# Kernel tuning notes

Measured on AMD Instinct MI355X. Metric: run time of the kernel, lower is better.

Reference implementation:

```python
import jax, jax.numpy as jnp
import numpy as np

D_MODEL = 512
NUM_HEADS = 8
HEAD_DIM = 64  # D_MODEL // NUM_HEADS


def setup_inputs() -> dict:
    key = jax.random.key(0)
    kq, kk, kv, kw, kb = jax.random.split(key, 5)
    B, S = 2, 2048
    query = jax.random.normal(kq, (B, S, D_MODEL), dtype=jnp.float32)
    key_t = jax.random.normal(kk, (B, S, D_MODEL), dtype=jnp.float32)
    value = jax.random.normal(kv, (B, S, D_MODEL), dtype=jnp.float32)
    # shared projection (nn.Linear(d_models, d_models)) applied to q, k, v
    scale = 1.0 / np.sqrt(D_MODEL)
    W = jax.random.uniform(kw, (D_MODEL, D_MODEL), dtype=jnp.float32, minval=-scale, maxval=scale)
    b = jax.random.uniform(kb, (D_MODEL,), dtype=jnp.float32, minval=-scale, maxval=scale)
    return {"query": query, "key": key_t, "value": value, "W": W, "b": b}


def reference(query, key, value, W, b):
    B, S, _ = query.shape
    H, Dh = NUM_HEADS, HEAD_DIM

    def proj(x):  # nn.Linear + ReLU, shared across q/k/v
        return jax.nn.relu(jnp.einsum('bsd,ed->bse', x, W) + b)

    # [B, S, d] -> [B, H, S, Dh]
    split = lambda x: proj(x).reshape(B, S, H, Dh).transpose(0, 2, 1, 3)
    Q, K, V = split(query), split(key), split(value)

    scores = jnp.einsum('bhqd,bhkd->bhqk', Q, K) / jnp.sqrt(jnp.float32(Dh))
    causal_mask = jnp.triu(jnp.ones((S, S), dtype=bool), k=1)  # True above diagonal
    scores = jnp.where(causal_mask, -jnp.inf, scores)
    attn = jax.nn.softmax(scores, axis=-1)
    out = jnp.einsum('bhqk,bhkd->bhqd', attn, V)  # [B, H, S, Dh]

    # faithful to original: transpose(0,1) swaps batch and heads, then view
    final = jnp.swapaxes(out, 0, 1).reshape(B, -1, D_MODEL)  # [B, S, d_model]
    return final
```

## Files before the change

### kernel.cpp

```cpp
#include <hip/hip_runtime.h>
#include <hip/hip_bf16.h>
#include <cstdint>
#include <cstddef>

typedef __bf16 bf16_t;
typedef bf16_t bf16x8 __attribute__((ext_vector_type(8)));
typedef float f32x4 __attribute__((ext_vector_type(4)));
typedef float f32x16 __attribute__((ext_vector_type(16)));
typedef unsigned short u16;
typedef u16 u16x8 __attribute__((ext_vector_type(8)));

#define S_LEN 2048
#define NB 2
#define NH 8
#define DHD 64
#define DM 512

static __device__ __forceinline__ u16 bfbits(float f) {
  union { __bf16 h; u16 u; } c; c.h = (__bf16)f; return c.u;
}
static __device__ __forceinline__ float bits2f(u16 b) {
  union { u16 u; __bf16 h; } c; c.u = b; return (float)c.h;
}
static __device__ __forceinline__ uint32_t pkbf(float a, float b) {
  union { __bf16 h[2]; uint32_t u; } c;
  c.h[0] = (__bf16)a; c.h[1] = (__bf16)b;
  return c.u;
}
static __device__ __forceinline__ void gload16(const void* g, void* l) {
  __builtin_amdgcn_global_load_lds(
      (const __attribute__((address_space(1))) uint32_t*)g,
      (__attribute__((address_space(3))) uint32_t*)l, 16, 0, 0);
}

static __device__ __forceinline__ int slot_of(int bh, int t32, int chunk) {
  int qb = t32 >> 2;
  int nc = (2 * (qb + 1) + 9) / 10;
  int off;
  if (qb < 10) off = (qb - 5) * 8;
  else if (qb < 15) off = 40 + (qb - 10) * 12;
  else off = 100;
  return bh * 116 + off + (t32 & 3) * nc + chunk;
}

__launch_bounds__(256, 3)
__global__ void proj_kernel(const float* __restrict__ Xq, const float* __restrict__ Xk,
                            const float* __restrict__ Xv, const float* __restrict__ W,
                            const float* __restrict__ bias,
                            u16* __restrict__ Qw, u16* __restrict__ Kw,
                            u16* __restrict__ Vt64) {
  __shared__ __align__(16) char pool[49152];
  float* AB[2]; float* BB[2];
  AB[0] = (float*)pool;
  AB[1] = AB[0] + 4096;
  BB[0] = AB[1] + 4096;
  BB[1] = BB[0] + 2048;

  const int bid = blockIdx.x;
  const int xcd = bid & 7;
  const int u = bid >> 3;
  const int n0 = (u & 7) * 64;
  const int mi = u >> 3;
  const int mg = (xcd * 12 + mi) * 128;
  const int z = mg >> 12;
  const int m_in = mg & 4095;
  const int b = m_in >> 11;
  const int s0m = m_in & (S_LEN - 1);
  const int hh = n0 >> 6;
  const float* __restrict__ X = (z == 0) ? Xq : ((z == 1) ? Xk : Xv);
  X += (size_t)m_in * DM;

  const int t = threadIdx.x;
  const int lane = t & 63;
  const int wid = t >> 6;
  const int wr = wid >> 1, wc = wid & 1;
  const int fr = lane & 15, fg = lane >> 4;

  f32x4 acc[4][2] = {};

  const int lrow = lane >> 3;
  const int lblk = lane & 7;

  auto stage = [&](int bf, int k0) {
    #pragma unroll
    for (int i = 0; i < 4; ++i) {
      int c = wid * 4 + i;
      int r = c * 8 + lrow;
      gload16(X + (size_t)r * DM + k0 + ((lblk ^ (r & 7)) << 2), AB[bf] + c * 256);
    }
    #pragma unroll
    for (int i = 0; i < 2; ++i) {
      int c = wid * 2 + i;
      int r = c * 8 + lrow;
      gload16(W + (size_t)(n0 + r) * DM + k0 + ((lblk ^ (r & 7)) << 2), BB[bf] + c * 256);
    }
  };

  stage(0, 0);
  int cb = 0;
  for (int t16 = 0; t16 < 16; ++t16) {
    __syncthreads();
    if (t16 < 15) stage(cb ^ 1, (t16 + 1) * 32);
    const float* Ac = AB[cb];
    const float* Bc = BB[cb];
    bf16x8 af[4], bfr[2];
    #pragma unroll
    for (int m2 = 0; m2 < 4; ++m2) {
      int r = wr*64 + m2*16 + fr;
      f32x4 lo = *(const f32x4*)&Ac[r*32 + (((2*fg)     ^ (r & 7)) << 2)];
      f32x4 hi = *(const f32x4*)&Ac[r*32 + (((2*fg + 1) ^ (r & 7)) << 2)];
      union { u16x8 s; bf16x8 v; } f;
      f.s[0]=bfbits(lo[0]); f.s[1]=bfbits(lo[1]); f.s[2]=bfbits(lo[2]); f.s[3]=bfbits(lo[3]);
      f.s[4]=bfbits(hi[0]); f.s[5]=bfbits(hi[1]); f.s[6]=bfbits(hi[2]); f.s[7]=bfbits(hi[3]);
      af[m2] = f.v;
    }
    #pragma unroll
    for (int ni = 0; ni < 2; ++ni) {
      int r = wc*32 + ni*16 + fr;
      f32x4 lo = *(const f32x4*)&Bc[r*32 + (((2*fg)     ^ (r & 7)) << 2)];
      f32x4 hi = *(const f32x4*)&Bc[r*32 + (((2*fg + 1) ^ (r & 7)) << 2)];
      union { u16x8 s; bf16x8 v; } f;
      f.s[0]=bfbits(lo[0]); f.s[1]=bfbits(lo[1]); f.s[2]=bfbits(lo[2]); f.s[3]=bfbits(lo[3]);
      f.s[4]=bfbits(hi[0]); f.s[5]=bfbits(hi[1]); f.s[6]=bfbits(hi[2]); f.s[7]=bfbits(hi[3]);
      bfr[ni] = f.v;
    }
    __builtin_amdgcn_s_setprio(1);
    #pragma unroll
    for (int m2 = 0; m2 < 4; ++m2)
      #pragma unroll
      for (int ni = 0; ni < 2; ++ni)
        acc[m2][ni] = __builtin_amdgcn_mfma_f32_16x16x32_bf16(af[m2], bfr[ni], acc[m2][ni], 0, 0, 0);
    __builtin_amdgcn_s_setprio(0);
    cb ^= 1;
  }
  __syncthreads();

  const float QSCALE = 0.125f * 1.44269504089f;
  const size_t bhh = (size_t)(b * NH + hh);
  u16* epi = (u16*)pool;

  if (z == 2) {
    #pragma unroll
    for (int m2 = 0; m2 < 4; ++m2) {
      #pragma unroll
      for (int ni = 0; ni < 2; ++ni) {
        int e = wc*32 + ni*16 + fr;
        int m = wr*64 + m2*16 + fg*4;
        float bv = bias[n0 + e];
        float v0 = fmaxf(acc[m2][ni][0] + bv, 0.f);
        float v1 = fmaxf(acc[m2][ni][1] + bv, 0.f);
        float v2 = fmaxf(acc[m2][ni][2] + bv, 0.f);
        float v3 = fmaxf(acc[m2][ni][3] + bv, 0.f);
        uint2 w; w.x = pkbf(v0, v1); w.y = pkbf(v2, v3);
        *(uint2*)&epi[e*136 + m] = w;
      }
    }
    __syncthreads();
    const int e = t >> 2, mc = (t & 3) * 32;
    const int sb = (s0m >> 6) + (mc >> 6);
    u16* dst = Vt64 + (((size_t)bhh * 32 + sb) * 64 + e) * 64 + (mc & 63);
    #pragma unroll
    for (int i = 0; i < 4; ++i)
      *(uint4*)(dst + i*8) = *(const uint4*)&epi[e*136 + mc + i*8];
  } else {
    #pragma unroll
    for (int m2 = 0; m2 < 4; ++m2) {
      #pragma unroll
      for (int ni = 0; ni < 2; ++ni) {
        int e = wc*32 + ni*16 + fr;
        float bv = bias[n0 + e];
        #pragma unroll
        for (int r = 0; r < 4; ++r) {
          float v = acc[m2][ni][r] + bv;
          if (z == 0) v *= QSCALE;
          v = fmaxf(v, 0.f);
          epi[(wr*64 + m2*16 + fg*4 + r)*72 + e] = bfbits(v);
        }
      }
    }
    __syncthreads();
    const int mrow = t >> 1, ec = (t & 1) * 32;
    u16* dst = ((z == 0) ? Qw : Kw) + (bhh * S_LEN + s0m + mrow) * DHD + ec;
    #pragma unroll
    for (int i = 0; i < 4; ++i)
      *(uint4*)(dst + i*8) = *(const uint4*)&epi[mrow*72 + ec + i*8];
  }
}

static __device__ const uint8_t QBT[34] = {4,5,6,7,8,9,9,10,10,11,11,12,12,13,13,14,14,14,15,15,15,
                                           3,8,13, 2,7,12, 1,6,11, 0,5,10,15};
static __device__ const uint8_t CKT[34] = {0,0,0,0,0,0,1,0,1,0,1,0,1,0,1,0,1,2,0,1,2,
                                           0,1,2, 0,1,2, 0,1,2, 0,1,2,3};

__launch_bounds__(256, 3)
__global__ void attn_kernel(const u16* __restrict__ Qw, const u16* __restrict__ Kw,
                            const u16* __restrict__ Vt64, u16* __restrict__ Opart,
                            float* __restrict__ lbuf, float* __restrict__ out) {
  __shared__ u16 KLDS[2][4096];
  __shared__ u16 VLDS[2][4096];
  const int t = threadIdx.x;
  const int lane = t & 63;
  const int wid = t >> 6;
  const int lam = lane & 31;
  const int hi = lane >> 5;
  const int h8 = hi << 3, h4 = hi << 2;
  const int bid = blockIdx.x;
  const int bh = bid & 15;
  const int u = bid >> 4;
  const int qb = QBT[u], chunk = CKT[u];
  const int steps_total = (qb + 1) * 2;
  const int sc0 = chunk * 10;
  const int sc1e = sc0 + 10;
  const int sc1 = (sc1e < steps_total) ? sc1e : steps_total;
  const int t32 = qb * 4 + wid;
  const int q0 = qb * 128 + wid * 32;

  const u16* __restrict__ Qh = Qw + (size_t)bh * S_LEN * DHD;
  const u16* __restrict__ Kh = Kw + (size_t)bh * S_LEN * DHD;
  const u16* __restrict__ V64 = Vt64 + (size_t)bh * 32 * 64 * 64;

  bf16x8 qf[4];
  #pragma unroll
  for (int c = 0; c < 4; ++c)
    qf[c] = *(const bf16x8*)(Qh + (size_t)(q0 + lam) * DHD + c*16 + h8);

  const int lrow = lane >> 3;
  const int lblk = lane & 7;
  auto stage = [&](int bf, int s) {
    #pragma unroll
    for (int i = 0; i < 2; ++i) {
      int c = wid * 2 + i;
      int r = c * 8 + lrow;
      int sw = (lblk ^ (r & 7)) << 3;
      gload16(Kh + (size_t)(s * 64 + r) * 64 + sw, &KLDS[bf][c * 512]);
      gload16(V64 + ((size_t)s * 64 + r) * 64 + sw, &VLDS[bf][c * 512]);
    }
  };

  f32x16 o0 = {}, o1 = {};
  float lsum = 0.f;

  auto softpack = [&](const f32x16& sc, bool msk, bf16x8& pb0v, bf16x8& pb1v) {
    float p[16];
    #pragma unroll
    for (int r = 0; r < 16; ++r) {
      float ev = __builtin_amdgcn_exp2f(sc[r]);
      int kc = (r & 3) + ((r >> 2) << 3) + h4;
      if (msk && kc > lam) ev = 0.f;
      p[r] = ev;
      lsum += ev;
    }
    uint32_t X0 = pkbf(p[0], p[1]),  X1 = pkbf(p[2], p[3]);
    uint32_t X2 = pkbf(p[4], p[5]),  X3 = pkbf(p[6], p[7]);
    uint32_t X4 = pkbf(p[8], p[9]),  X5 = pkbf(p[10], p[11]);
    uint32_t X6 = pkbf(p[12], p[13]), X7 = pkbf(p[14], p[15]);
    asm("v_permlane32_swap_b32 %0, %1" : "+v"(X0), "+v"(X2));
    asm("v_permlane32_swap_b32 %0, %1" : "+v"(X1), "+v"(X3));
    asm("v_permlane32_swap_b32 %0, %1" : "+v"(X4), "+v"(X6));
    asm("v_permlane32_swap_b32 %0, %1" : "+v"(X5), "+v"(X7));
    union U8 { uint32_t u[4]; bf16x8 v; };
    U8 a, bU;
    a.u[0] = X0; a.u[1] = X1; a.u[2] = X2; a.u[3] = X3;
    bU.u[0] = X4; bU.u[1] = X5; bU.u[2] = X6; bU.u[3] = X7;
    pb0v = a.v; pb1v = bU.v;
  };

  stage(0, sc0);
  int cb = 0;
  for (int s = sc0; s < sc1; ++s) {
    __syncthreads();
    if (s + 1 < sc1) stage(cb ^ 1, s + 1);
    const int d2 = t32 - 2 * s;
    bf16x8 a0, a1, b0v, b1v;
    f32x16 sA = {}, sB = {};
    if (d2 >= 0) {
      bf16x8 kA[4];
      #pragma unroll
      for (int c = 0; c < 4; ++c) {
        int r = lam, e = ((2*c + hi) ^ (r & 7)) * 8;
        kA[c] = *(const bf16x8*)&KLDS[cb][r*64 + e];
      }
      __builtin_amdgcn_s_setprio(1);
      #pragma unroll
      for (int c = 0; c < 4; ++c)
        sA = __builtin_amdgcn_mfma_f32_32x32x16_bf16(kA[c], qf[c], sA, 0, 0, 0);
      __builtin_amdgcn_s_setprio(0);
    }
    if (d2 >= 1) {
      bf16x8 kB[4];
      #pragma unroll
      for (int c = 0; c < 4; ++c) {
        int r = 32 + lam, e = ((2*c + hi) ^ (r & 7)) * 8;
        kB[c] = *(const bf16x8*)&KLDS[cb][r*64 + e];
      }
      __builtin_amdgcn_s_setprio(1);
      #pragma unroll
      for (int c = 0; c < 4; ++c)
        sB = __builtin_amdgcn_mfma_f32_32x32x16_bf16(kB[c], qf[c], sB, 0, 0, 0);
      __builtin_amdgcn_s_setprio(0);
    }
    if (d2 >= 0) softpack(sA, d2 == 0, a0, a1);
    if (d2 >= 1) softpack(sB, d2 == 1, b0v, b1v);
    if (d2 >= 0) {
      bf16x8 v0[2], v1[2];
      #pragma unroll
      for (int c2 = 0; c2 < 2; ++c2) {
        int r0 = lam,      e0 = ((2*c2 + hi) ^ (r0 & 7)) * 8;
        int r1 = 32 + lam, e1 = ((2*c2 + hi) ^ (r1 & 7)) * 8;
        v0[c2] = *(const bf16x8*)&VLDS[cb][r0*64 + e0];
        v1[c2] = *(const bf16x8*)&VLDS[cb][r1*64 + e1];
      }
      __builtin_amdgcn_s_setprio(1);
      o0 = __builtin_amdgcn_mfma_f32_32x32x16_bf16(v0[0], a0, o0, 0, 0, 0);
      o0 = __builtin_amdgcn_mfma_f32_32x32x16_bf16(v0[1], a1, o0, 0, 0, 0);
      o1 = __builtin_amdgcn_mfma_f32_32x32x16_bf16(v1[0], a0, o1, 0, 0, 0);
      o1 = __builtin_amdgcn_mfma_f32_32x32x16_bf16(v1[1], a1, o1, 0, 0, 0);
      __builtin_amdgcn_s_setprio(0);
    }
    if (d2 >= 1) {
      bf16x8 v0[2], v1[2];
      #pragma unroll
      for (int c2 = 0; c2 < 2; ++c2) {
        int r0 = lam,      e0 = ((4 + 2*c2 + hi) ^ (r0 & 7)) * 8;
        int r1 = 32 + lam, e1 = ((4 + 2*c2 + hi) ^ (r1 & 7)) * 8;
        v0[c2] = *(const bf16x8*)&VLDS[cb][r0*64 + e0];
        v1[c2] = *(const bf16x8*)&VLDS[cb][r1*64 + e1];
      }
      __builtin_amdgcn_s_setprio(1);
      o0 = __builtin_amdgcn_mfma_f32_32x32x16_bf16(v0[0], b0v, o0, 0, 0, 0);
      o0 = __builtin_amdgcn_mfma_f32_32x32x16_bf16(v0[1], b1v, o0, 0, 0, 0);
      o1 = __builtin_amdgcn_mfma_f32_32x32x16_bf16(v1[0], b0v, o1, 0, 0, 0);
      o1 = __builtin_amdgcn_mfma_f32_32x32x16_bf16(v1[1], b1v, o1, 0, 0, 0);
      __builtin_amdgcn_s_setprio(0);
    }
    cb ^= 1;
  }

  float l = lsum + __shfl_xor(lsum, 32);

  if (qb <= 4) {
    const int b = bh >> 3, hh = bh & 7;
    const float inv = 1.0f / l;
    float* orow = out + (((size_t)(hh * NB + b)) * S_LEN + (q0 + lam)) * DHD;
    #pragma unroll
    for (int r = 0; r < 16; ++r) {
      int d = (r & 3) + ((r >> 2) << 3) + h4;
      orow[d] = o0[r] * inv;
      orow[d + 32] = o1[r] * inv;
    }
  } else {
    const int slot = slot_of(bh, t32, chunk);
    uint32_t w[16] __attribute__((aligned(16)));
    #pragma unroll
    for (int m = 0; m < 8; ++m) {
      w[m]     = pkbf(o0[2*m], o0[2*m+1]);
      w[8 + m] = pkbf(o1[2*m], o1[2*m+1]);
    }
    u16* op = Opart + (size_t)slot * 2048 + (size_t)lane * 32;
    #pragma unroll
    for (int i = 0; i < 4; ++i)
      *(uint4*)(op + i*8) = *(const uint4*)&w[i*4];
    if (lane < 32) lbuf[slot * 32 + lane] = l;
  }
}

__launch_bounds__(256)
__global__ void reduce_kernel(const u16* __restrict__ Opart,
                              const float* __restrict__ lbuf,
                              float* __restrict__ out) {
  const int t = threadIdx.x;
  const int unit = blockIdx.x * 4 + (t >> 6);
  const int bh = unit & 15;
  const int ti = 20 + (unit >> 4);
  const int qb = ti >> 2;
  const int nc = (2 * (qb + 1) + 9) / 10;
  const int lane = t & 63;
  const int lam = lane & 31;
  const int h4 = (lane >> 5) << 2;
  const int slot0 = slot_of(bh, ti, 0);

  float O[32];
  #pragma unroll
  for (int i = 0; i < 32; ++i) O[i] = 0.f;
  float L = 0.f;

  for (int c = 0; c < nc; ++c) {
    const u16* op = Opart + (size_t)(slot0 + c) * 2048 + (size_t)lane * 32;
    L += lbuf[(slot0 + c) * 32 + lam];
    #pragma unroll
    for (int i = 0; i < 4; ++i) {
      uint4 v = *(const uint4*)(op + i*8);
      uint32_t a[4] = {v.x, v.y, v.z, v.w};
      #pragma unroll
      for (int jj = 0; jj < 4; ++jj) {
        O[i*8 + 2*jj]     += bits2f((u16)(a[jj] & 0xFFFFu));
        O[i*8 + 2*jj + 1] += bits2f((u16)(a[jj] >> 16));
      }
    }
  }

  const int b = bh >> 3, hh = bh & 7;
  const float inv = 1.0f / L;
  float* orow = out + (((size_t)(hh * NB + b)) * S_LEN + (ti*32 + lam)) * DHD;
  #pragma unroll
  for (int r = 0; r < 16; ++r) {
    int d = (r & 3) + ((r >> 2) << 3) + h4;
    orow[d] = O[r] * inv;
    orow[d + 32] = O[16 + r] * inv;
  }
}

extern "C" void kernel_launch(void* const* d_in, const int* in_sizes, int n_in,
                              void* d_out, int out_size, void* d_ws, size_t ws_size,
                              hipStream_t stream) {
  const float* q = (const float*)d_in[0];
  const float* k = (const float*)d_in[1];
  const float* v = (const float*)d_in[2];
  const float* W = (const float*)d_in[3];
  const float* b = (const float*)d_in[4];

  const size_t elems = (size_t)NB * NH * S_LEN * DHD;
  u16* Qw = (u16*)d_ws;
  u16* Kw = Qw + elems;
  u16* Vt64 = Kw + elems;
  u16* Opart = Vt64 + elems;
  float* lbuf = (float*)(Opart + (size_t)1856 * 2048);

  proj_kernel<<<dim3(768), dim3(256), 0, stream>>>(q, k, v, W, b, Qw, Kw, Vt64);

  attn_kernel<<<dim3(544), dim3(256), 0, stream>>>(Qw, Kw, Vt64, Opart, lbuf, (float*)d_out);

  reduce_kernel<<<dim3(176), dim3(256), 0, stream>>>(Opart, lbuf, (float*)d_out);
}
```

Measured before the change: 51.21 us.

## Pre-convert inputs and weight to bf16 and deepen the projection load pipeline

Adds a separate conversion kernel that turns q, k, v and W from fp32 into bf16 in workspace. The projection GEMM then stages bf16 tiles straight into LDS and skips the per-iteration fp32-to-bf16 conversion. Its LDS ring grows from two to four buffers, three stages in flight, with explicit vmcnt waits. The cost is an extra kernel launch plus a full fp32 read and bf16 write of all inputs. Opart is now aliased onto the converted-input buffer, which is safe because projection has finished before attention writes it.

```diff
diff --git a/kernel.cpp b/kernel.cpp
--- a/kernel.cpp
+++ b/kernel.cpp
@@ -43,19 +43,29 @@
   return bh * 116 + off + (t32 & 3) * nc + chunk;
 }
 
+__launch_bounds__(256)
+__global__ void cvt_kernel(const float* __restrict__ q, const float* __restrict__ k,
+                           const float* __restrict__ v, const float* __restrict__ W,
+                           u16* __restrict__ dst) {
+  const int z = blockIdx.y;
+  if (z == 3 && blockIdx.x >= 128) return;
+  const float* __restrict__ src = (z == 0) ? q : (z == 1) ? k : (z == 2) ? v : W;
+  u16* __restrict__ d = dst + (size_t)z * 2097152;
+  size_t i = ((size_t)blockIdx.x * 256 + threadIdx.x) * 8;
+  float4 a = *reinterpret_cast<const float4*>(src + i);
+  float4 b = *reinterpret_cast<const float4*>(src + i + 4);
+  u16x8 r;
+  r[0] = bfbits(a.x); r[1] = bfbits(a.y); r[2] = bfbits(a.z); r[3] = bfbits(a.w);
+  r[4] = bfbits(b.x); r[5] = bfbits(b.y); r[6] = bfbits(b.z); r[7] = bfbits(b.w);
+  *reinterpret_cast<u16x8*>(d + i) = r;
+}
+
 __launch_bounds__(256, 3)
-__global__ void proj_kernel(const float* __restrict__ Xq, const float* __restrict__ Xk,
-                            const float* __restrict__ Xv, const float* __restrict__ W,
+__global__ void proj_kernel(const u16* __restrict__ Xall, const u16* __restrict__ Wb,
                             const float* __restrict__ bias,
                             u16* __restrict__ Qw, u16* __restrict__ Kw,
                             u16* __restrict__ Vt64) {
-  __shared__ __align__(16) char pool[49152];
-  float* AB[2]; float* BB[2];
-  AB[0] = (float*)pool;
-  AB[1] = AB[0] + 4096;
-  BB[0] = AB[1] + 4096;
-  BB[1] = BB[0] + 2048;
-
+  __shared__ __align__(16) u16 BUF[4][6144];
   const int bid = blockIdx.x;
   const int xcd = bid & 7;
   const int u = bid >> 3;
@@ -67,8 +77,7 @@
   const int b = m_in >> 11;
   const int s0m = m_in & (S_LEN - 1);
   const int hh = n0 >> 6;
-  const float* __restrict__ X = (z == 0) ? Xq : ((z == 1) ? Xk : Xv);
-  X += (size_t)m_in * DM;
+  const u16* __restrict__ X = Xall + (size_t)z * 2097152 + (size_t)m_in * DM;
 
   const int t = threadIdx.x;
   const int lane = t & 63;
@@ -78,51 +87,44 @@
 
   f32x4 acc[4][2] = {};
 
-  const int lrow = lane >> 3;
-  const int lblk = lane & 7;
+  const int lrow = lane >> 2;
+  const int lblk = lane & 3;
 
   auto stage = [&](int bf, int k0) {
-    #pragma unroll
-    for (int i = 0; i < 4; ++i) {
-      int c = wid * 4 + i;
-      int r = c * 8 + lrow;
-      gload16(X + (size_t)r * DM + k0 + ((lblk ^ (r & 7)) << 2), AB[bf] + c * 256);
-    }
     #pragma unroll
     for (int i = 0; i < 2; ++i) {
       int c = wid * 2 + i;
-      int r = c * 8 + lrow;
-      gload16(W + (size_t)(n0 + r) * DM + k0 + ((lblk ^ (r & 7)) << 2), BB[bf] + c * 256);
+      int r = c * 16 + lrow;
+      gload16(X + (size_t)r * DM + k0 + ((lblk ^ (r & 3)) << 3), &BUF[bf][c * 512]);
+    }
+    {
+      int r = wid * 16 + lrow;
+      gload16(Wb + (size_t)(n0 + r) * DM + k0 + ((lblk ^ (r & 3)) << 3),
+              &BUF[bf][4096 + wid * 512]);
     }
   };
 
   stage(0, 0);
-  int cb = 0;
-  for (int t16 = 0; t16 < 16; ++t16) {
-    __syncthreads();
-    if (t16 < 15) stage(cb ^ 1, (t16 + 1) * 32);
-    const float* Ac = AB[cb];
-    const float* Bc = BB[cb];
+  stage(1, 32);
+  stage(2, 64);
+  for (int i = 0; i < 16; ++i) {
+    if (i < 14)      asm volatile("s_waitcnt vmcnt(6)" ::: "memory");
+    else if (i == 14) asm volatile("s_waitcnt vmcnt(3)" ::: "memory");
+    else              asm volatile("s_waitcnt vmcnt(0)" ::: "memory");
+    __builtin_amdgcn_s_barrier();
+    __builtin_amdgcn_sched_barrier(0);
+    if (i + 3 < 16) stage((i + 3) & 3, (i + 3) * 32);
+    const u16* Bc = &BUF[i & 3][0];
     bf16x8 af[4], bfr[2];
     #pragma unroll
     for (int m2 = 0; m2 < 4; ++m2) {
       int r = wr*64 + m2*16 + fr;
-      f32x4 lo = *(const f32x4*)&Ac[r*32 + (((2*fg)     ^ (r & 7)) << 2)];
-      f32x4 hi = *(const f32x4*)&Ac[r*32 + (((2*fg + 1) ^ (r & 7)) << 2)];
-      union { u16x8 s; bf16x8 v; } f;
-      f.s[0]=bfbits(lo[0]); f.s[1]=bfbits(lo[1]); f.s[2]=bfbits(lo[2]); f.s[3]=bfbits(lo[3]);
-      f.s[4]=bfbits(hi[0]); f.s[5]=bfbits(hi[1]); f.s[6]=bfbits(hi[2]); f.s[7]=bfbits(hi[3]);
-      af[m2] = f.v;
+      af[m2] = *(const bf16x8*)&Bc[r*32 + ((fg ^ (r & 3)) << 3)];
     }
     #pragma unroll
     for (int ni = 0; ni < 2; ++ni) {
       int r = wc*32 + ni*16 + fr;
-      f32x4 lo = *(const f32x4*)&Bc[r*32 + (((2*fg)     ^ (r & 7)) << 2)];
-      f32x4 hi = *(const f32x4*)&Bc[r*32 + (((2*fg + 1) ^ (r & 7)) << 2)];
-      union { u16x8 s; bf16x8 v; } f;
-      f.s[0]=bfbits(lo[0]); f.s[1]=bfbits(lo[1]); f.s[2]=bfbits(lo[2]); f.s[3]=bfbits(lo[3]);
-      f.s[4]=bfbits(hi[0]); f.s[5]=bfbits(hi[1]); f.s[6]=bfbits(hi[2]); f.s[7]=bfbits(hi[3]);
-      bfr[ni] = f.v;
+      bfr[ni] = *(const bf16x8*)&Bc[4096 + r*32 + ((fg ^ (r & 3)) << 3)];
     }
     __builtin_amdgcn_s_setprio(1);
     #pragma unroll
@@ -131,13 +133,12 @@
       for (int ni = 0; ni < 2; ++ni)
         acc[m2][ni] = __builtin_amdgcn_mfma_f32_16x16x32_bf16(af[m2], bfr[ni], acc[m2][ni], 0, 0, 0);
     __builtin_amdgcn_s_setprio(0);
-    cb ^= 1;
   }
   __syncthreads();
 
   const float QSCALE = 0.125f * 1.44269504089f;
   const size_t bhh = (size_t)(b * NH + hh);
-  u16* epi = (u16*)pool;
+  u16* epi = &BUF[0][0];
 
   if (z == 2) {
     #pragma unroll
@@ -423,10 +424,14 @@
   u16* Qw = (u16*)d_ws;
   u16* Kw = Qw + elems;
   u16* Vt64 = Kw + elems;
-  u16* Opart = Vt64 + elems;
-  float* lbuf = (float*)(Opart + (size_t)1856 * 2048);
-
-  proj_kernel<<<dim3(768), dim3(256), 0, stream>>>(q, k, v, W, b, Qw, Kw, Vt64);
+  u16* Xb = Vt64 + elems;
+  u16* Wb = Xb + 3 * elems;
+  u16* Opart = Xb;
+  float* lbuf = (float*)(Wb + 262144);
+
+  cvt_kernel<<<dim3(1024, 4), dim3(256), 0, stream>>>(q, k, v, W, Xb);
+
+  proj_kernel<<<dim3(768), dim3(256), 0, stream>>>(Xb, Wb, b, Qw, Kw, Vt64);
 
   attn_kernel<<<dim3(544), dim3(256), 0, stream>>>(Qw, Kw, Vt64, Opart, lbuf, (float*)d_out);
 
```

Result: slower. 57.45 us (+12.2%).

## Triple-buffer LDS staging with explicit vmcnt waits in projection and attention

Applied to the files above, without the earlier changes.

Both kernels move from double-buffered LDS tiles to a three-deep ring that is filled two steps ahead. The full __syncthreads is replaced by an s_waitcnt vmcnt on outstanding async global-to-LDS loads followed by a bare s_barrier. The goal is to hide more global load latency behind the MFMA work. In exchange, LDS use grows (72KB in proj, so its launch bound drops from 3 to 2 blocks, and 48KB in attn), and the hard-coded vmcnt counts must exactly match the number of loads each stage issues. The attention prologue also stages the second step unconditionally, even when a chunk has only one step.

```diff
diff --git a/kernel.cpp b/kernel.cpp
--- a/kernel.cpp
+++ b/kernel.cpp
@@ -43,19 +43,13 @@
   return bh * 116 + off + (t32 & 3) * nc + chunk;
 }
 
-__launch_bounds__(256, 3)
+__launch_bounds__(256, 2)
 __global__ void proj_kernel(const float* __restrict__ Xq, const float* __restrict__ Xk,
                             const float* __restrict__ Xv, const float* __restrict__ W,
                             const float* __restrict__ bias,
                             u16* __restrict__ Qw, u16* __restrict__ Kw,
                             u16* __restrict__ Vt64) {
-  __shared__ __align__(16) char pool[49152];
-  float* AB[2]; float* BB[2];
-  AB[0] = (float*)pool;
-  AB[1] = AB[0] + 4096;
-  BB[0] = AB[1] + 4096;
-  BB[1] = BB[0] + 2048;
-
+  __shared__ __align__(16) float BUF[3][6144];
   const int bid = blockIdx.x;
   const int xcd = bid & 7;
   const int u = bid >> 3;
@@ -86,23 +80,26 @@
     for (int i = 0; i < 4; ++i) {
       int c = wid * 4 + i;
       int r = c * 8 + lrow;
-      gload16(X + (size_t)r * DM + k0 + ((lblk ^ (r & 7)) << 2), AB[bf] + c * 256);
+      gload16(X + (size_t)r * DM + k0 + ((lblk ^ (r & 7)) << 2), &BUF[bf][c * 256]);
     }
     #pragma unroll
     for (int i = 0; i < 2; ++i) {
       int c = wid * 2 + i;
       int r = c * 8 + lrow;
-      gload16(W + (size_t)(n0 + r) * DM + k0 + ((lblk ^ (r & 7)) << 2), BB[bf] + c * 256);
+      gload16(W + (size_t)(n0 + r) * DM + k0 + ((lblk ^ (r & 7)) << 2),
+              &BUF[bf][4096 + c * 256]);
     }
   };
 
   stage(0, 0);
-  int cb = 0;
-  for (int t16 = 0; t16 < 16; ++t16) {
-    __syncthreads();
-    if (t16 < 15) stage(cb ^ 1, (t16 + 1) * 32);
-    const float* Ac = AB[cb];
-    const float* Bc = BB[cb];
+  stage(1, 32);
+  int cur = 0;
+  for (int i = 0; i < 16; ++i) {
+    if (i < 15) asm volatile("s_waitcnt vmcnt(6)" ::: "memory");
+    else        asm volatile("s_waitcnt vmcnt(0)" ::: "memory");
+    __builtin_amdgcn_s_barrier();
+    if (i < 14) { int nb = cur + 2; if (nb >= 3) nb -= 3; stage(nb, (i + 2) * 32); }
+    const float* Ac = BUF[cur];
     bf16x8 af[4], bfr[2];
     #pragma unroll
     for (int m2 = 0; m2 < 4; ++m2) {
@@ -117,8 +114,8 @@
     #pragma unroll
     for (int ni = 0; ni < 2; ++ni) {
       int r = wc*32 + ni*16 + fr;
-      f32x4 lo = *(const f32x4*)&Bc[r*32 + (((2*fg)     ^ (r & 7)) << 2)];
-      f32x4 hi = *(const f32x4*)&Bc[r*32 + (((2*fg + 1) ^ (r & 7)) << 2)];
+      f32x4 lo = *(const f32x4*)&Ac[4096 + r*32 + (((2*fg)     ^ (r & 7)) << 2)];
+      f32x4 hi = *(const f32x4*)&Ac[4096 + r*32 + (((2*fg + 1) ^ (r & 7)) << 2)];
       union { u16x8 s; bf16x8 v; } f;
       f.s[0]=bfbits(lo[0]); f.s[1]=bfbits(lo[1]); f.s[2]=bfbits(lo[2]); f.s[3]=bfbits(lo[3]);
       f.s[4]=bfbits(hi[0]); f.s[5]=bfbits(hi[1]); f.s[6]=bfbits(hi[2]); f.s[7]=bfbits(hi[3]);
@@ -131,13 +128,13 @@
       for (int ni = 0; ni < 2; ++ni)
         acc[m2][ni] = __builtin_amdgcn_mfma_f32_16x16x32_bf16(af[m2], bfr[ni], acc[m2][ni], 0, 0, 0);
     __builtin_amdgcn_s_setprio(0);
-    cb ^= 1;
+    cur = (cur + 1 == 3) ? 0 : cur + 1;
   }
   __syncthreads();
 
   const float QSCALE = 0.125f * 1.44269504089f;
   const size_t bhh = (size_t)(b * NH + hh);
-  u16* epi = (u16*)pool;
+  u16* epi = (u16*)&BUF[0][0];
 
   if (z == 2) {
     #pragma unroll
@@ -196,8 +193,8 @@
 __global__ void attn_kernel(const u16* __restrict__ Qw, const u16* __restrict__ Kw,
                             const u16* __restrict__ Vt64, u16* __restrict__ Opart,
                             float* __restrict__ lbuf, float* __restrict__ out) {
-  __shared__ u16 KLDS[2][4096];
-  __shared__ u16 VLDS[2][4096];
+  __shared__ u16 KLDS[3][4096];
+  __shared__ u16 VLDS[3][4096];
   const int t = threadIdx.x;
   const int lane = t & 63;
   const int wid = t >> 6;
@@ -266,10 +263,13 @@
   };
 
   stage(0, sc0);
-  int cb = 0;
+  stage(1, sc0 + 1);
+  int cur = 0;
   for (int s = sc0; s < sc1; ++s) {
-    __syncthreads();
-    if (s + 1 < sc1) stage(cb ^ 1, s + 1);
+    if (s + 1 < sc1) asm volatile("s_waitcnt vmcnt(4)" ::: "memory");
+    else             asm volatile("s_waitcnt vmcnt(0)" ::: "memory");
+    __builtin_amdgcn_s_barrier();
+    if (s + 2 < sc1) { int nb = cur + 2; if (nb >= 3) nb -= 3; stage(nb, s + 2); }
     const int d2 = t32 - 2 * s;
     bf16x8 a0, a1, b0v, b1v;
     f32x16 sA = {}, sB = {};
@@ -278,7 +278,7 @@
       #pragma unroll
       for (int c = 0; c < 4; ++c) {
         int r = lam, e = ((2*c + hi) ^ (r & 7)) * 8;
-        kA[c] = *(const bf16x8*)&KLDS[cb][r*64 + e];
+        kA[c] = *(const bf16x8*)&KLDS[cur][r*64 + e];
       }
       __builtin_amdgcn_s_setprio(1);
       #pragma unroll
@@ -291,7 +291,7 @@
       #pragma unroll
       for (int c = 0; c < 4; ++c) {
         int r = 32 + lam, e = ((2*c + hi) ^ (r & 7)) * 8;
-        kB[c] = *(const bf16x8*)&KLDS[cb][r*64 + e];
+        kB[c] = *(const bf16x8*)&KLDS[cur][r*64 + e];
       }
       __builtin_amdgcn_s_setprio(1);
       #pragma unroll
@@ -307,8 +307,8 @@
       for (int c2 = 0; c2 < 2; ++c2) {
         int r0 = lam,      e0 = ((2*c2 + hi) ^ (r0 & 7)) * 8;
         int r1 = 32 + lam, e1 = ((2*c2 + hi) ^ (r1 & 7)) * 8;
-        v0[c2] = *(const bf16x8*)&VLDS[cb][r0*64 + e0];
-        v1[c2] = *(const bf16x8*)&VLDS[cb][r1*64 + e1];
+        v0[c2] = *(const bf16x8*)&VLDS[cur][r0*64 + e0];
+        v1[c2] = *(const bf16x8*)&VLDS[cur][r1*64 + e1];
       }
       __builtin_amdgcn_s_setprio(1);
       o0 = __builtin_amdgcn_mfma_f32_32x32x16_bf16(v0[0], a0, o0, 0, 0, 0);
@@ -323,8 +323,8 @@
       for (int c2 = 0; c2 < 2; ++c2) {
         int r0 = lam,      e0 = ((4 + 2*c2 + hi) ^ (r0 & 7)) * 8;
         int r1 = 32 + lam, e1 = ((4 + 2*c2 + hi) ^ (r1 & 7)) * 8;
-        v0[c2] = *(const bf16x8*)&VLDS[cb][r0*64 + e0];
-        v1[c2] = *(const bf16x8*)&VLDS[cb][r1*64 + e1];
+        v0[c2] = *(const bf16x8*)&VLDS[cur][r0*64 + e0];
+        v1[c2] = *(const bf16x8*)&VLDS[cur][r1*64 + e1];
       }
       __builtin_amdgcn_s_setprio(1);
       o0 = __builtin_amdgcn_mfma_f32_32x32x16_bf16(v0[0], b0v, o0, 0, 0, 0);
@@ -333,7 +333,7 @@
       o1 = __builtin_amdgcn_mfma_f32_32x32x16_bf16(v1[1], b1v, o1, 0, 0, 0);
       __builtin_amdgcn_s_setprio(0);
     }
-    cb ^= 1;
+    cur = (cur + 1 == 3) ? 0 : cur + 1;
   }
 
   float l = lsum + __shfl_xor(lsum, 32);
```

Result: slower. 53.75 us (+4.9%).

## Widen projection GEMM tile to 128x128 to halve block count

Applied to the files above, without the earlier changes.

The projection kernel's output tile grows from 128x64 to 128x128, so each block covers two heads and the grid shrinks from 768 to 384 blocks. The intent is to raise arithmetic intensity and reuse each X tile across twice as many output columns, cutting redundant global loads of the fp32 activations. In exchange, LDS per block grows to 64KB and accumulator registers double, so launch bounds drop to 2 blocks per CU. With fewer blocks there is also less parallelism over the 256 CUs.

```diff
diff --git a/kernel.cpp b/kernel.cpp
--- a/kernel.cpp
+++ b/kernel.cpp
@@ -43,30 +43,24 @@
   return bh * 116 + off + (t32 & 3) * nc + chunk;
 }
 
-__launch_bounds__(256, 3)
+__launch_bounds__(256, 2)
 __global__ void proj_kernel(const float* __restrict__ Xq, const float* __restrict__ Xk,
                             const float* __restrict__ Xv, const float* __restrict__ W,
                             const float* __restrict__ bias,
                             u16* __restrict__ Qw, u16* __restrict__ Kw,
                             u16* __restrict__ Vt64) {
-  __shared__ __align__(16) char pool[49152];
-  float* AB[2]; float* BB[2];
-  AB[0] = (float*)pool;
-  AB[1] = AB[0] + 4096;
-  BB[0] = AB[1] + 4096;
-  BB[1] = BB[0] + 2048;
-
+  __shared__ __align__(16) float BUF[2][8192];
   const int bid = blockIdx.x;
   const int xcd = bid & 7;
   const int u = bid >> 3;
-  const int n0 = (u & 7) * 64;
-  const int mi = u >> 3;
-  const int mg = (xcd * 12 + mi) * 128;
+  const int n0 = (u & 3) * 128;
+  const int mIdx = u >> 2;
+  const int mg = (xcd * 12 + mIdx) * 128;
   const int z = mg >> 12;
   const int m_in = mg & 4095;
   const int b = m_in >> 11;
   const int s0m = m_in & (S_LEN - 1);
-  const int hh = n0 >> 6;
+  const int h0 = n0 >> 6;
   const float* __restrict__ X = (z == 0) ? Xq : ((z == 1) ? Xk : Xv);
   X += (size_t)m_in * DM;
 
@@ -76,7 +70,7 @@
   const int wr = wid >> 1, wc = wid & 1;
   const int fr = lane & 15, fg = lane >> 4;
 
-  f32x4 acc[4][2] = {};
+  f32x4 acc[4][4] = {};
 
   const int lrow = lane >> 3;
   const int lblk = lane & 7;
@@ -86,24 +80,24 @@
     for (int i = 0; i < 4; ++i) {
       int c = wid * 4 + i;
       int r = c * 8 + lrow;
-      gload16(X + (size_t)r * DM + k0 + ((lblk ^ (r & 7)) << 2), AB[bf] + c * 256);
-    }
-    #pragma unroll
-    for (int i = 0; i < 2; ++i) {
-      int c = wid * 2 + i;
+      gload16(X + (size_t)r * DM + k0 + ((lblk ^ (r & 7)) << 2), &BUF[bf][c * 256]);
+    }
+    #pragma unroll
+    for (int i = 0; i < 4; ++i) {
+      int c = wid * 4 + i;
       int r = c * 8 + lrow;
-      gload16(W + (size_t)(n0 + r) * DM + k0 + ((lblk ^ (r & 7)) << 2), BB[bf] + c * 256);
+      gload16(W + (size_t)(n0 + r) * DM + k0 + ((lblk ^ (r & 7)) << 2),
+              &BUF[bf][4096 + c * 256]);
     }
   };
 
   stage(0, 0);
   int cb = 0;
-  for (int t16 = 0; t16 < 16; ++t16) {
+  for (int i = 0; i < 16; ++i) {
     __syncthreads();
-    if (t16 < 15) stage(cb ^ 1, (t16 + 1) * 32);
-    const float* Ac = AB[cb];
-    const float* Bc = BB[cb];
-    bf16x8 af[4], bfr[2];
+    if (i < 15) stage(cb ^ 1, (i + 1) * 32);
+    const float* Ac = BUF[cb];
+    bf16x8 af[4], bfr[4];
     #pragma unroll
     for (int m2 = 0; m2 < 4; ++m2) {
       int r = wr*64 + m2*16 + fr;
@@ -115,10 +109,10 @@
       af[m2] = f.v;
     }
     #pragma unroll
-    for (int ni = 0; ni < 2; ++ni) {
-      int r = wc*32 + ni*16 + fr;
-      f32x4 lo = *(const f32x4*)&Bc[r*32 + (((2*fg)     ^ (r & 7)) << 2)];
-      f32x4 hi = *(const f32x4*)&Bc[r*32 + (((2*fg + 1) ^ (r & 7)) << 2)];
+    for (int ni = 0; ni < 4; ++ni) {
+      int r = wc*64 + ni*16 + fr;
+      f32x4 lo = *(const f32x4*)&Ac[4096 + r*32 + (((2*fg)     ^ (r & 7)) << 2)];
+      f32x4 hi = *(const f32x4*)&Ac[4096 + r*32 + (((2*fg + 1) ^ (r & 7)) << 2)];
       union { u16x8 s; bf16x8 v; } f;
       f.s[0]=bfbits(lo[0]); f.s[1]=bfbits(lo[1]); f.s[2]=bfbits(lo[2]); f.s[3]=bfbits(lo[3]);
       f.s[4]=bfbits(hi[0]); f.s[5]=bfbits(hi[1]); f.s[6]=bfbits(hi[2]); f.s[7]=bfbits(hi[3]);
@@ -128,7 +122,7 @@
     #pragma unroll
     for (int m2 = 0; m2 < 4; ++m2)
       #pragma unroll
-      for (int ni = 0; ni < 2; ++ni)
+      for (int ni = 0; ni < 4; ++ni)
         acc[m2][ni] = __builtin_amdgcn_mfma_f32_16x16x32_bf16(af[m2], bfr[ni], acc[m2][ni], 0, 0, 0);
     __builtin_amdgcn_s_setprio(0);
     cb ^= 1;
@@ -136,15 +130,14 @@
   __syncthreads();
 
   const float QSCALE = 0.125f * 1.44269504089f;
-  const size_t bhh = (size_t)(b * NH + hh);
-  u16* epi = (u16*)pool;
+  u16* epi = (u16*)&BUF[0][0];
 
   if (z == 2) {
     #pragma unroll
     for (int m2 = 0; m2 < 4; ++m2) {
       #pragma unroll
-      for (int ni = 0; ni < 2; ++ni) {
-        int e = wc*32 + ni*16 + fr;
+      for (int ni = 0; ni < 4; ++ni) {
+        int e = wc*64 + ni*16 + fr;
         int m = wr*64 + m2*16 + fg*4;
         float bv = bias[n0 + e];
         float v0 = fmaxf(acc[m2][ni][0] + bv, 0.f);
@@ -156,34 +149,36 @@
       }
     }
     __syncthreads();
-    const int e = t >> 2, mc = (t & 3) * 32;
+    const int e2 = t >> 1, mc = (t & 1) * 64;
+    const int h = h0 + (e2 >> 6), d = e2 & 63;
     const int sb = (s0m >> 6) + (mc >> 6);
-    u16* dst = Vt64 + (((size_t)bhh * 32 + sb) * 64 + e) * 64 + (mc & 63);
-    #pragma unroll
-    for (int i = 0; i < 4; ++i)
-      *(uint4*)(dst + i*8) = *(const uint4*)&epi[e*136 + mc + i*8];
+    u16* dst = Vt64 + (((size_t)(b * NH + h) * 32 + sb) * 64 + d) * 64;
+    #pragma unroll
+    for (int i = 0; i < 8; ++i)
+      *(uint4*)(dst + i*8) = *(const uint4*)&epi[e2*136 + mc + i*8];
   } else {
     #pragma unroll
     for (int m2 = 0; m2 < 4; ++m2) {
       #pragma unroll
-      for (int ni = 0; ni < 2; ++ni) {
-        int e = wc*32 + ni*16 + fr;
+      for (int ni = 0; ni < 4; ++ni) {
+        int e = wc*64 + ni*16 + fr;
         float bv = bias[n0 + e];
         #pragma unroll
         for (int r = 0; r < 4; ++r) {
           float v = acc[m2][ni][r] + bv;
           if (z == 0) v *= QSCALE;
           v = fmaxf(v, 0.f);
-          epi[(wr*64 + m2*16 + fg*4 + r)*72 + e] = bfbits(v);
+          epi[(wr*64 + m2*16 + fg*4 + r)*136 + e] = bfbits(v);
         }
       }
     }
     __syncthreads();
-    const int mrow = t >> 1, ec = (t & 1) * 32;
-    u16* dst = ((z == 0) ? Qw : Kw) + (bhh * S_LEN + s0m + mrow) * DHD + ec;
-    #pragma unroll
-    for (int i = 0; i < 4; ++i)
-      *(uint4*)(dst + i*8) = *(const uint4*)&epi[mrow*72 + ec + i*8];
+    const int mrow = t >> 1, hf = t & 1;
+    u16* dst = ((z == 0) ? Qw : Kw) +
+               (((size_t)(b * NH + h0 + hf)) * S_LEN + s0m + mrow) * DHD;
+    #pragma unroll
+    for (int i = 0; i < 8; ++i)
+      *(uint4*)(dst + i*8) = *(const uint4*)&epi[mrow*136 + hf*64 + i*8];
   }
 }
 
@@ -426,7 +421,7 @@
   u16* Opart = Vt64 + elems;
   float* lbuf = (float*)(Opart + (size_t)1856 * 2048);
 
-  proj_kernel<<<dim3(768), dim3(256), 0, stream>>>(q, k, v, W, b, Qw, Kw, Vt64);
+  proj_kernel<<<dim3(384), dim3(256), 0, stream>>>(q, k, v, W, b, Qw, Kw, Vt64);
 
   attn_kernel<<<dim3(544), dim3(256), 0, stream>>>(Qw, Kw, Vt64, Opart, lbuf, (float*)d_out);
 
```

Result: no change. 50.51 us, median of 2 (-1.4%).
